# Optimization experiments

Hardware: AMD Instinct MI355X
Metric: run time of the kernel (lower is better)

## Reference

```python
import jax, jax.numpy as jnp
import numpy as np

REL_LEN = 100  # self.relative_length in the module
LN_EPS = 1e-3  # tf.keras LayerNormalization default epsilon


def sinusoid_table(rel_len, d):
    # position_encoding_relative: sinusoid over relative offsets -L..L, [2L+1, d]
    pos = jnp.arange(-rel_len, rel_len + 1, dtype=jnp.float32)[:, None]
    i = jnp.arange(d // 2, dtype=jnp.float32)[None, :]
    inv_freq = jnp.exp(-jnp.log(10000.0) * (2.0 * i) / d)
    ang = pos * inv_freq
    return jnp.concatenate([jnp.sin(ang), jnp.cos(ang)], axis=-1)


def setup_inputs() -> dict:
    key = jax.random.key(0)
    B, S, E, HID, H = 4, 512, 512, 2048, 8
    ks = jax.random.split(key, 16)
    g = lambda k, sh: jax.random.normal(k, sh, jnp.float32) / jnp.sqrt(jnp.float32(sh[0]))
    return {
        "values": jax.random.normal(ks[0], (B, S, E), jnp.float32),
        "values_mask": jnp.ones((B, S), dtype=bool),
        "rel_enc": sinusoid_table(REL_LEN, E),            # [201, E]
        "ln0_g": jnp.ones((E,), jnp.float32), "ln0_b": jnp.zeros((E,), jnp.float32),
        "w_b0": g(ks[1], (E, HID)), "b_b0": jnp.zeros((HID,), jnp.float32),
        "wq": g(ks[2], (HID, E)), "bq": jnp.zeros((E,), jnp.float32),
        "wke": g(ks[3], (HID, E)), "bke": jnp.zeros((E,), jnp.float32),
        "wkv": g(ks[4], (HID, E)), "bkv": jnp.zeros((E,), jnp.float32),
        "wkr": g(ks[5], (E, E)), "bkr": jnp.zeros((E,), jnp.float32),
        "wab0": g(ks[6], (E, H)), "bab0": jnp.zeros((H,), jnp.float32),
        "wab1": g(ks[7], (E, H)), "bab1": jnp.zeros((H,), jnp.float32),
        "ln1_g": jnp.ones((E,), jnp.float32), "ln1_b": jnp.zeros((E,), jnp.float32),
        "w11": g(ks[8], (E, HID)), "b11": jnp.zeros((HID,), jnp.float32),
        "w12": g(ks[9], (HID, E)), "b12": jnp.zeros((E,), jnp.float32),
    }


def _ln(x, g, b):
    m = jnp.mean(x, -1, keepdims=True)
    v = jnp.var(x, -1, keepdims=True)
    return (x - m) * jax.lax.rsqrt(v + LN_EPS) * g + b


def reference(values, values_mask, rel_enc, ln0_g, ln0_b, w_b0, b_b0,
              wq, bq, wke, bke, wkv, bkv, wkr, bkr,
              wab0, bab0, wab1, bab1, ln1_g, ln1_b, w11, b11, w12, b12):
    B, S, E = values.shape
    H = wab0.shape[1]
    D = E // H
    # block0 (lastfc=False): LayerNorm -> Dense(hidden, relu)
    x = jax.nn.relu(_ln(values, ln0_g, ln0_b) @ w_b0 + b_b0)          # [B,S,HID]
    q = x @ wq + bq                                                    # [B,S,E]
    ke = x @ wke + bke
    kv = x @ wkv + bkv
    # relative encodings: gather = one-hot rel map @ encoding table
    offs = jnp.clip(jnp.arange(S)[None, :] - jnp.arange(S)[:, None], -REL_LEN, REL_LEN) + REL_LEN
    rel = rel_enc[offs]                                                # [S,S,E]
    kr = rel @ wkr + bkr                                               # [S,S,E]
    # learned bias terms
    bias0 = (ke @ wab0 + bab0).transpose(0, 2, 1)[:, :, None, :]       # [B,H,1,S]
    bias1 = (kr @ wab1 + bab1).transpose(2, 0, 1)[None]                # [1,H,S,S]
    tr = lambda u: u.reshape(B, S, H, D).transpose(0, 2, 1, 3)         # [B,H,S,D]
    qh, keh, kvh = tr(q), tr(ke), tr(kv)
    krh = kr.reshape(S, S, H, D).transpose(2, 0, 1, 3)                 # [H,S,S,D]
    # q . kr content-position term, contracted without [B,H,S,S,D] materialization
    biasprod = jnp.einsum('bhid,hijd->bhij', qh, krh)                  # [B,H,S,S]
    bias = biasprod + bias0 + bias1
    # AttentionWithBias: scaled dot product + bias, key mask + causal mask
    logits = jnp.einsum('bhid,bhjd->bhij', qh, keh) / jnp.sqrt(jnp.float32(D)) + bias
    causal = jnp.tril(jnp.ones((S, S), dtype=bool))[None, None]        # [1,1,S,S]
    keymask = values_mask[:, None, None, :]                            # [B,1,1,S]
    logits = jnp.where(causal & keymask, logits, jnp.float32(-1e9))
    scores = jax.nn.softmax(logits, axis=-1)
    att = jnp.einsum('bhij,bhjd->bhid', scores, kvh)                   # [B,H,S,D]
    att = att.transpose(0, 2, 1, 3).reshape(B, S, E)
    v = values + att
    # block1: LayerNorm -> Dense(hidden, relu) -> Dense(input_size)
    y = jax.nn.relu(_ln(v, ln1_g, ln1_b) @ w11 + b11) @ w12 + b12
    return v + y
```

## Files before the change

### kernel.cpp

```cpp
#include <hip/hip_runtime.h>
#include <hip/hip_bf16.h>
#include <cstddef>
#include <cstdint>

#define LN_EPS 0.001f

using short8 = __attribute__((ext_vector_type(8))) short;
using f32x4 = __attribute__((ext_vector_type(4))) float;

#define GLOAD_LDS16(gp, lp)                                                    \
  __builtin_amdgcn_global_load_lds(                                            \
      (const __attribute__((address_space(1))) void*)(gp),                     \
      (__attribute__((address_space(3))) void*)(lp), 16, 0, 0)

static __device__ __forceinline__ short f2bf(float x) {
  __hip_bfloat16 h = __float2bfloat16(x);
  return *reinterpret_cast<short*>(&h);
}

__global__ __launch_bounds__(256) void prep_ln_kernel(
    const float* __restrict__ w_b0, const float* __restrict__ w11,
    const float* __restrict__ wq, const float* __restrict__ wke,
    const float* __restrict__ wkv, const float* __restrict__ w12,
    const float* __restrict__ wkr, const float* __restrict__ rel_enc,
    __hip_bfloat16* __restrict__ w_b0t, __hip_bfloat16* __restrict__ w11t,
    __hip_bfloat16* __restrict__ wqt, __hip_bfloat16* __restrict__ wket,
    __hip_bfloat16* __restrict__ wkvt, __hip_bfloat16* __restrict__ w12t,
    __hip_bfloat16* __restrict__ wkrt, __hip_bfloat16* __restrict__ relb,
    const float* __restrict__ lnx, const float* __restrict__ lng,
    const float* __restrict__ lnb, __hip_bfloat16* __restrict__ lnout,
    const float* __restrict__ bab0, const float* __restrict__ bab1,
    float* __restrict__ keab, float* __restrict__ b1t) {
  int bid = blockIdx.x;
  int t = threadIdx.x;
  if (bid >= 8768) {
    int idx = (bid - 8768) * 256 + t;
    if (idx < 208 * 8) b1t[idx] = bab1[idx & 7];
    return;
  }
  if (bid >= 8704) {
    int idx = (bid - 8704) * 256 + t;
    keab[idx] = bab0[(idx >> 9) & 7];
    return;
  }
  if (bid >= 6656) {
    int row = bid - 6656;
    const float* xr = lnx + (size_t)row * 512;
    float v0 = xr[t], v1 = xr[t + 256];
    float s = v0 + v1, sq = v0 * v0 + v1 * v1;
#pragma unroll
    for (int o = 32; o; o >>= 1) {
      s += __shfl_down(s, o);
      sq += __shfl_down(sq, o);
    }
    __shared__ float wsum[4], wsq[4];
    __shared__ float mean_s, scale_s;
    int wid = t >> 6, lane = t & 63;
    if (lane == 0) { wsum[wid] = s; wsq[wid] = sq; }
    __syncthreads();
    if (t == 0) {
      float S = wsum[0] + wsum[1] + wsum[2] + wsum[3];
      float SQ = wsq[0] + wsq[1] + wsq[2] + wsq[3];
      float mean = S * (1.f / 512.f);
      float var = SQ * (1.f / 512.f) - mean * mean;
      mean_s = mean;
      scale_s = rsqrtf(var + LN_EPS);
    }
    __syncthreads();
    float mean = mean_s, scale = scale_s;
    __hip_bfloat16* orow = lnout + (size_t)row * 512;
    orow[t] = __float2bfloat16((v0 - mean) * scale * lng[t] + lnb[t]);
    orow[t + 256] = __float2bfloat16((v1 - mean) * scale * lng[t + 256] + lnb[t + 256]);
    return;
  }
  if (bid >= 6400) {
    int row = bid - 6400;
    float v0 = 0.f, v1 = 0.f;
    if (row < 201) {
      v0 = rel_enc[(size_t)row * 512 + t];
      v1 = rel_enc[(size_t)row * 512 + t + 256];
    }
    relb[(size_t)row * 512 + t] = __float2bfloat16(v0);
    relb[(size_t)row * 512 + t + 256] = __float2bfloat16(v1);
    return;
  }
  const float* in;
  __hip_bfloat16* outp;
  int R, C, bx, by;
  if (bid < 6144) {
    int seg = bid >> 10, idx = bid & 1023;
    if (seg == 0)      { in = w_b0; outp = w_b0t; R = 512;  C = 2048; }
    else if (seg == 1) { in = w11;  outp = w11t;  R = 512;  C = 2048; }
    else if (seg == 2) { in = wq;   outp = wqt;   R = 2048; C = 512;  }
    else if (seg == 3) { in = wke;  outp = wket;  R = 2048; C = 512;  }
    else if (seg == 4) { in = wkv;  outp = wkvt;  R = 2048; C = 512;  }
    else               { in = w12;  outp = w12t;  R = 2048; C = 512;  }
    if (R == 512) { bx = idx & 63; by = idx >> 6; }
    else          { bx = idx & 15; by = idx >> 4; }
  } else {
    int idx = bid - 6144;
    in = wkr; outp = wkrt; R = 512; C = 512;
    bx = idx & 15; by = idx >> 4;
  }
  __shared__ float tile[32][33];
  int c0 = bx * 32, r0 = by * 32;
  int tx = t & 31, ty = t >> 5;
#pragma unroll
  for (int p = 0; p < 4; p++) {
    int r = ty + p * 8;
    tile[r][tx] = in[(size_t)(r0 + r) * C + c0 + tx];
  }
  __syncthreads();
#pragma unroll
  for (int p = 0; p < 4; p++) {
    int r = ty + p * 8;
    outp[(size_t)(c0 + r) * R + r0 + tx] = __float2bfloat16(tile[tx][r]);
  }
}

__global__ __launch_bounds__(256) void ln_kernel(const float* __restrict__ x,
                                                 const float* __restrict__ g,
                                                 const float* __restrict__ bb,
                                                 __hip_bfloat16* __restrict__ out) {
  int row = blockIdx.x;
  const float* xr = x + (size_t)row * 512;
  int t = threadIdx.x;
  float v0 = xr[t], v1 = xr[t + 256];
  float s = v0 + v1, sq = v0 * v0 + v1 * v1;
#pragma unroll
  for (int o = 32; o; o >>= 1) {
    s += __shfl_down(s, o);
    sq += __shfl_down(sq, o);
  }
  __shared__ float wsum[4], wsq[4];
  __shared__ float mean_s, scale_s;
  int wid = t >> 6, lane = t & 63;
  if (lane == 0) { wsum[wid] = s; wsq[wid] = sq; }
  __syncthreads();
  if (t == 0) {
    float S = wsum[0] + wsum[1] + wsum[2] + wsum[3];
    float SQ = wsq[0] + wsq[1] + wsq[2] + wsq[3];
    float mean = S * (1.f / 512.f);
    float var = SQ * (1.f / 512.f) - mean * mean;
    mean_s = mean;
    scale_s = rsqrtf(var + LN_EPS);
  }
  __syncthreads();
  float mean = mean_s, scale = scale_s;
  __hip_bfloat16* orow = out + (size_t)row * 512;
  orow[t] = __float2bfloat16((v0 - mean) * scale * g[t] + bb[t]);
  orow[t + 256] = __float2bfloat16((v1 - mean) * scale * g[t + 256] + bb[t + 256]);
}

template <int TM, int TN, int MODE, int RELU, int RESID, int DOT>
__global__ __launch_bounds__(256) void gemm_mfma(
    const __hip_bfloat16* __restrict__ A, const __hip_bfloat16* __restrict__ Bt,
    const float* __restrict__ bias0, const float* __restrict__ bias1,
    const float* __restrict__ bias2, const float* __restrict__ resid,
    void* __restrict__ out0, void* __restrict__ out1, void* __restrict__ out2,
    int M, int N, int K,
    const __hip_bfloat16* A2, const __hip_bfloat16* B2t,
    const float* bias_kr, void* out_kr, int ysplit,
    const float* wdot0, float* dot0, const float* wdot1, float* dot1) {
  constexpr int FM = TM / 32;
  constexpr int FN = TN / 32;
  __shared__ short As[2][TM * 64];
  __shared__ short Bs[2][TN * 64];
  int tid = threadIdx.x;
  int w = tid >> 6, lane = tid & 63;
  int wrow = (w >> 1) * (TM / 2);
  int wcol = (w & 1) * (TN / 2);
  int quad = lane >> 4, l16 = lane & 15;
  int bx = blockIdx.x, by = blockIdx.y;
  const short* Ag = (const short*)A;
  const short* Bg = (const short*)Bt;
  int N_ = N, K_ = K;
  bool is_kr = false;
  if (MODE == 1 && ysplit > 0 && by >= ysplit) {
    if (bx >= 512 / TN) return;
    is_kr = true;
    by -= ysplit;
    Ag = (const short*)A2;
    Bg = (const short*)B2t;
    N_ = 512;
    K_ = 512;
  }
  int row0 = by * TM, col0 = bx * TN;
  f32x4 acc[FM][FN];
#pragma unroll
  for (int i = 0; i < FM; i++)
#pragma unroll
    for (int j = 0; j < FN; j++) acc[i][j] = {0.f, 0.f, 0.f, 0.f};

  auto stage = [&](int k0, int buf) {
#pragma unroll
    for (int p = 0; p < TM / 32; p++) {
      int e = p * 256 + tid;
      int r = e >> 3, sc = e & 7;
      int c = sc ^ (r & 7);
      GLOAD_LDS16(Ag + (size_t)(row0 + r) * K_ + k0 + c * 8, &As[buf][e * 8]);
    }
#pragma unroll
    for (int p = 0; p < TN / 32; p++) {
      int e = p * 256 + tid;
      int r = e >> 3, sc = e & 7;
      int c = sc ^ (r & 7);
      GLOAD_LDS16(Bg + (size_t)(col0 + r) * K_ + k0 + c * 8, &Bs[buf][e * 8]);
    }
  };

  int nIter = K_ >> 6;
  stage(0, 0);
  for (int it = 0; it < nIter; ++it) {
    int cur = it & 1;
    __syncthreads();
    if (it + 1 < nIter) stage((it + 1) << 6, cur ^ 1);
#pragma unroll
    for (int u = 0; u < 2; u++) {
      short8 af[FM], bf[FN];
#pragma unroll
      for (int f = 0; f < FM; f++) {
        int r = wrow + f * 16 + l16;
        int slot = (u * 4 + quad) ^ (r & 7);
        af[f] = *(const short8*)&As[cur][(r * 8 + slot) * 8];
      }
#pragma unroll
      for (int f = 0; f < FN; f++) {
        int r = wcol + f * 16 + l16;
        int slot = (u * 4 + quad) ^ (r & 7);
        bf[f] = *(const short8*)&Bs[cur][(r * 8 + slot) * 8];
      }
#pragma unroll
      for (int fm = 0; fm < FM; fm++)
#pragma unroll
        for (int fn = 0; fn < FN; fn++)
          acc[fm][fn] = __builtin_amdgcn_mfma_f32_16x16x32_bf16(af[fm], bf[fn], acc[fm][fn], 0, 0, 0);
    }
  }

  if (MODE == 2) {
    int seg = col0 >> 9;
    const float* bp = (seg == 0) ? bias0 : (seg == 1 ? bias1 : bias2);
    if (seg < 2) {
      __hip_bfloat16* dst = (__hip_bfloat16*)(seg == 0 ? out0 : out1);
#pragma unroll
      for (int fm = 0; fm < FM; fm++) {
#pragma unroll
        for (int r = 0; r < 4; r++) {
          int gr = row0 + wrow + fm * 16 + quad * 4 + r;
          float dotp[8] = {0.f, 0.f, 0.f, 0.f, 0.f, 0.f, 0.f, 0.f};
#pragma unroll
          for (int fn = 0; fn < FN; fn++) {
            int gc = col0 + wcol + fn * 16 + l16;
            int bcol = gc - seg * 512;
            float v = acc[fm][fn][r] + bp[bcol];
            dst[(size_t)gr * 512 + bcol] = __float2bfloat16(v);
            if (DOT && seg == 1) {
              const float4* wv = (const float4*)&wdot0[(size_t)bcol * 8];
              float4 w0 = wv[0], w1 = wv[1];
              dotp[0] += v * w0.x; dotp[1] += v * w0.y; dotp[2] += v * w0.z; dotp[3] += v * w0.w;
              dotp[4] += v * w1.x; dotp[5] += v * w1.y; dotp[6] += v * w1.z; dotp[7] += v * w1.w;
            }
          }
          if (DOT && seg == 1) {
#pragma unroll
            for (int h = 0; h < 8; h++) {
              float d = dotp[h];
              d += __shfl_xor(d, 1);
              d += __shfl_xor(d, 2);
              d += __shfl_xor(d, 4);
              d += __shfl_xor(d, 8);
              if (l16 == 0) {
                int b_ = gr >> 9, s_ = gr & 511;
                atomicAdd(&dot0[(size_t)(b_ * 8 + h) * 512 + s_], d);
              }
            }
          }
        }
      }
    } else {
#pragma unroll
      for (int fm = 0; fm < FM; fm++) {
#pragma unroll
        for (int fn = 0; fn < FN; fn++) {
          int gc = col0 + wcol + fn * 16 + l16;
          int bcol = gc - 1024;
          float bv = bp[bcol];
          int gr0 = row0 + wrow + fm * 16 + quad * 4;
          union { unsigned long long u; short s4[4]; } pk;
#pragma unroll
          for (int r = 0; r < 4; r++) pk.s4[r] = f2bf(acc[fm][fn][r] + bv);
          int b_ = gr0 >> 9, s_ = gr0 & 511;
          int h_ = bcol >> 6, d_ = bcol & 63;
          *(unsigned long long*)&((short*)out2)[(size_t)((b_ * 8 + h_) * 64 + d_) * 512 + s_] = pk.u;
        }
      }
    }
  } else if (MODE == 1) {
    const float* bp = is_kr ? bias_kr : bias0;
    __hip_bfloat16* dst = is_kr ? (__hip_bfloat16*)out_kr : (__hip_bfloat16*)out0;
#pragma unroll
    for (int fm = 0; fm < FM; fm++) {
#pragma unroll
      for (int r = 0; r < 4; r++) {
        int gr = row0 + wrow + fm * 16 + quad * 4 + r;
        float dotp[8] = {0.f, 0.f, 0.f, 0.f, 0.f, 0.f, 0.f, 0.f};
#pragma unroll
        for (int fn = 0; fn < FN; fn++) {
          int gc = col0 + wcol + fn * 16 + l16;
          float v = acc[fm][fn][r] + bp[gc];
          if (RELU && !is_kr) v = fmaxf(v, 0.f);
          dst[(size_t)gr * N_ + gc] = __float2bfloat16(v);
          if (DOT && is_kr) {
            const float4* wv = (const float4*)&wdot1[(size_t)gc * 8];
            float4 w0 = wv[0], w1 = wv[1];
            dotp[0] += v * w0.x; dotp[1] += v * w0.y; dotp[2] += v * w0.z; dotp[3] += v * w0.w;
            dotp[4] += v * w1.x; dotp[5] += v * w1.y; dotp[6] += v * w1.z; dotp[7] += v * w1.w;
          }
        }
        if (DOT && is_kr) {
#pragma unroll
          for (int h = 0; h < 8; h++) {
            float d = dotp[h];
            d += __shfl_xor(d, 1);
            d += __shfl_xor(d, 2);
            d += __shfl_xor(d, 4);
            d += __shfl_xor(d, 8);
            if (l16 == 0 && gr < 208) atomicAdd(&dot1[gr * 8 + h], d);
          }
        }
      }
    }
  } else {
#pragma unroll
    for (int fm = 0; fm < FM; fm++) {
#pragma unroll
      for (int fn = 0; fn < FN; fn++) {
        int gc = col0 + wcol + fn * 16 + l16;
        float bv = bias0[gc];
#pragma unroll
        for (int r = 0; r < 4; r++) {
          int gr = row0 + wrow + fm * 16 + quad * 4 + r;
          float v = acc[fm][fn][r] + bv;
          if (RELU) v = fmaxf(v, 0.f);
          size_t idx = (size_t)gr * N_ + gc;
          if (RESID) v += resid[idx];
          ((float*)out0)[idx] = v;
        }
      }
    }
  }
}

#define PST 136
__global__ __launch_bounds__(256) void attn_mfma4(
    const __hip_bfloat16* __restrict__ q, const __hip_bfloat16* __restrict__ ke,
    const __hip_bfloat16* __restrict__ kvt, const __hip_bfloat16* __restrict__ krtb,
    const float* __restrict__ keab, const float* __restrict__ b1t,
    const float* __restrict__ values, float* __restrict__ v_out) {
  const int S = 512, E = 512;
  __shared__ float bp[16 * 113];
  __shared__ short P[4][16 * PST];
  __shared__ float ml[4][32];
  int tid = threadIdx.x;
  int wave = tid >> 6, lane = tid & 63;
  int quad = lane >> 4, l16 = lane & 15;
  int band = 31 - blockIdx.x;
  int h = blockIdx.y, b = blockIdx.z;
  int wi0 = band * 16;

  const short* qg = (const short*)q;
  const short* keg = (const short*)ke;
  const short* kvtg = (const short*)kvt;
  const short* krg = (const short*)krtb;

  short8 aq[2];
#pragma unroll
  for (int kk = 0; kk < 2; kk++)
    aq[kk] = *(const short8*)&qg[(size_t)(b * S + wi0 + l16) * E + h * 64 + kk * 32 + quad * 8];

#pragma unroll
  for (int oi = 0; oi < 2; oi++) {
    int on = wave + oi * 4;
    if (on < 7) {
      f32x4 c = {0.f, 0.f, 0.f, 0.f};
#pragma unroll
      for (int kk = 0; kk < 2; kk++) {
        short8 bfr = *(const short8*)&krg[(size_t)(on * 16 + l16) * E + h * 64 + kk * 32 + quad * 8];
        c = __builtin_amdgcn_mfma_f32_16x16x32_bf16(aq[kk], bfr, c, 0, 0, 0);
      }
      float b1 = b1t[(on * 16 + l16) * 8 + h];
#pragma unroll
      for (int rr = 0; rr < 4; rr++)
        bp[(quad * 4 + rr) * 113 + on * 16 + l16] = c[rr] + b1;
    }
  }
  __syncthreads();

  int nb = (band >= wave) ? (((band - wave) >> 2) + 1) : 0;

  f32x4 s[8];
  const float* keabh = keab + (size_t)(b * 8 + h) * 512;
#pragma unroll
  for (int t = 0; t < 8; t++) {
    if (t < nb) {
      int j = (4 * t + wave) * 16 + l16;
      f32x4 c = {0.f, 0.f, 0.f, 0.f};
#pragma unroll
      for (int kk = 0; kk < 2; kk++) {
        short8 bk = *(const short8*)&keg[(size_t)(b * S + j) * E + h * 64 + kk * 32 + quad * 8];
        c = __builtin_amdgcn_mfma_f32_16x16x32_bf16(aq[kk], bk, c, 0, 0, 0);
      }
      float ka = keabh[j];
#pragma unroll
      for (int rr = 0; rr < 4; rr++) {
        int i = wi0 + quad * 4 + rr;
        float val = -1e30f;
        if (j <= i) {
          int off = j - i + 100;
          if (off < 0) off = 0;
          val = c[rr] * 0.125f + bp[(quad * 4 + rr) * 113 + off] + ka;
        }
        s[t][rr] = val;
      }
    }
  }

  float m_r[4] = {-1e30f, -1e30f, -1e30f, -1e30f};
#pragma unroll
  for (int t = 0; t < 8; t++)
    if (t < nb)
#pragma unroll
      for (int rr = 0; rr < 4; rr++) m_r[rr] = fmaxf(m_r[rr], s[t][rr]);
#pragma unroll
  for (int rr = 0; rr < 4; rr++) {
    float v = m_r[rr];
    v = fmaxf(v, __shfl_xor(v, 1));
    v = fmaxf(v, __shfl_xor(v, 2));
    v = fmaxf(v, __shfl_xor(v, 4));
    v = fmaxf(v, __shfl_xor(v, 8));
    m_r[rr] = v;
  }
  float l_r[4] = {0.f, 0.f, 0.f, 0.f};
  short* Pw = &P[wave][0];
#pragma unroll
  for (int t = 0; t < 8; t++) {
    if (t < nb) {
#pragma unroll
      for (int rr = 0; rr < 4; rr++) {
        float p = __expf(s[t][rr] - m_r[rr]);
        l_r[rr] += p;
        Pw[(quad * 4 + rr) * PST + t * 16 + l16] = f2bf(p);
      }
    }
  }
  if (nb & 1) {
#pragma unroll
    for (int rr = 0; rr < 4; rr++)
      Pw[(quad * 4 + rr) * PST + nb * 16 + l16] = 0;
  }
#pragma unroll
  for (int rr = 0; rr < 4; rr++) {
    float v = l_r[rr];
    v += __shfl_xor(v, 1);
    v += __shfl_xor(v, 2);
    v += __shfl_xor(v, 4);
    v += __shfl_xor(v, 8);
    l_r[rr] = v;
  }

  f32x4 o[4] = {{0.f,0.f,0.f,0.f},{0.f,0.f,0.f,0.f},{0.f,0.f,0.f,0.f},{0.f,0.f,0.f,0.f}};
  int nkk = (nb + 1) >> 1;
  const short* kvbase = &kvtg[(size_t)(b * 8 + h) * 64 * S];
#pragma unroll
  for (int kk = 0; kk < 4; kk++) {
    if (kk < nkk) {
      short8 ap = *(const short8*)&Pw[l16 * PST + kk * 32 + quad * 8];
      int jgl = (4 * (2 * kk + (quad >> 1)) + wave) * 16 + (quad & 1) * 8;
#pragma unroll
      for (int dn = 0; dn < 4; dn++) {
        short8 bv = *(const short8*)&kvbase[(size_t)(dn * 16 + l16) * S + jgl];
        o[dn] = __builtin_amdgcn_mfma_f32_16x16x32_bf16(ap, bv, o[dn], 0, 0, 0);
      }
    }
  }

  float* omw = (float*)&P[wave][0];
#pragma unroll
  for (int rr = 0; rr < 4; rr++) {
    int row = quad * 4 + rr;
    if (l16 == 0) {
      ml[wave][row * 2] = m_r[rr];
      ml[wave][row * 2 + 1] = l_r[rr];
    }
#pragma unroll
    for (int dn = 0; dn < 4; dn++)
      omw[row * 68 + dn * 16 + l16] = o[dn][rr];
  }
  __syncthreads();
  int dn = wave;
#pragma unroll
  for (int rr = 0; rr < 4; rr++) {
    int row = quad * 4 + rr;
    float ms = -1e30f;
#pragma unroll
    for (int wv = 0; wv < 4; wv++) ms = fmaxf(ms, ml[wv][row * 2]);
    float lsum = 0.f, oo = 0.f;
    int col = dn * 16 + l16;
#pragma unroll
    for (int wv = 0; wv < 4; wv++) {
      float aw = __expf(ml[wv][row * 2] - ms);
      lsum += ml[wv][row * 2 + 1] * aw;
      oo += ((float*)&P[wv][0])[row * 68 + col] * aw;
    }
    oo /= lsum;
    size_t idx = (size_t)(b * S + wi0 + row) * E + h * 64 + col;
    v_out[idx] = values[idx] + oo;
  }
}

extern "C" void kernel_launch(void* const* d_in, const int* in_sizes, int n_in,
                              void* d_out, int out_size, void* d_ws, size_t ws_size,
                              hipStream_t stream) {
  const float* values = (const float*)d_in[0];
  const float* rel_enc = (const float*)d_in[2];
  const float* ln0_g = (const float*)d_in[3];
  const float* ln0_b = (const float*)d_in[4];
  const float* w_b0 = (const float*)d_in[5];
  const float* b_b0 = (const float*)d_in[6];
  const float* wq = (const float*)d_in[7];
  const float* bq = (const float*)d_in[8];
  const float* wke = (const float*)d_in[9];
  const float* bke = (const float*)d_in[10];
  const float* wkv = (const float*)d_in[11];
  const float* bkv = (const float*)d_in[12];
  const float* wkr = (const float*)d_in[13];
  const float* bkr = (const float*)d_in[14];
  const float* wab0 = (const float*)d_in[15];
  const float* bab0 = (const float*)d_in[16];
  const float* wab1 = (const float*)d_in[17];
  const float* bab1 = (const float*)d_in[18];
  const float* ln1_g = (const float*)d_in[19];
  const float* ln1_b = (const float*)d_in[20];
  const float* w11 = (const float*)d_in[21];
  const float* b11 = (const float*)d_in[22];
  const float* w12 = (const float*)d_in[23];
  const float* b12 = (const float*)d_in[24];
  float* out = (float*)d_out;

  char* p = (char*)d_ws;
  __hip_bfloat16* buf_ln = (__hip_bfloat16*)p;  p += (size_t)2048 * 512 * 2;
  __hip_bfloat16* x      = (__hip_bfloat16*)p;  p += (size_t)2048 * 2048 * 2;
  __hip_bfloat16* q      = (__hip_bfloat16*)p;  p += (size_t)2048 * 512 * 2;
  __hip_bfloat16* ke     = (__hip_bfloat16*)p;  p += (size_t)2048 * 512 * 2;
  __hip_bfloat16* kvt    = (__hip_bfloat16*)p;  p += (size_t)2048 * 512 * 2;
  float* v    = (float*)p;                      p += (size_t)2048 * 512 * 4;
  __hip_bfloat16* krtb = (__hip_bfloat16*)p;    p += (size_t)256 * 512 * 2;
  __hip_bfloat16* relb = (__hip_bfloat16*)p;    p += (size_t)256 * 512 * 2;
  __hip_bfloat16* wkrt = (__hip_bfloat16*)p;    p += (size_t)512 * 512 * 2;
  float* keab = (float*)p;                      p += (size_t)4 * 8 * 512 * 4;
  float* b1t  = (float*)p;                      p += (size_t)208 * 8 * 4;
  __hip_bfloat16* w_b0t = (__hip_bfloat16*)p;   p += (size_t)2048 * 512 * 2;
  __hip_bfloat16* wcatt = (__hip_bfloat16*)p;   p += (size_t)1536 * 2048 * 2;
  __hip_bfloat16* w11t  = (__hip_bfloat16*)p;   p += (size_t)2048 * 512 * 2;
  __hip_bfloat16* w12t  = (__hip_bfloat16*)p;   p += (size_t)512 * 2048 * 2;

  __hip_bfloat16* wqt  = wcatt;
  __hip_bfloat16* wket = wcatt + (size_t)512 * 2048;
  __hip_bfloat16* wkvt = wcatt + (size_t)1024 * 2048;

  prep_ln_kernel<<<8775, 256, 0, stream>>>(w_b0, w11, wq, wke, wkv, w12, wkr, rel_enc,
                                           w_b0t, w11t, wqt, wket, wkvt, w12t, wkrt, relb,
                                           values, ln0_g, ln0_b, buf_ln,
                                           bab0, bab1, keab, b1t);
  gemm_mfma<128, 64, 1, 1, 0, 1><<<dim3(32, 18), 256, 0, stream>>>(
      buf_ln, w_b0t, b_b0, nullptr, nullptr, nullptr, x, nullptr, nullptr,
      2048, 2048, 512, relb, wkrt, bkr, krtb, 16,
      nullptr, nullptr, wab1, b1t);
  gemm_mfma<128, 64, 2, 0, 0, 1><<<dim3(24, 16), 256, 0, stream>>>(
      x, wcatt, bq, bke, bkv, nullptr, q, ke, kvt, 2048, 1536, 2048,
      nullptr, nullptr, nullptr, nullptr, 0,
      wab0, keab, nullptr, nullptr);
  attn_mfma4<<<dim3(32, 8, 4), 256, 0, stream>>>(q, ke, kvt, krtb, keab, b1t, values, v);
  ln_kernel<<<2048, 256, 0, stream>>>(v, ln1_g, ln1_b, buf_ln);
  gemm_mfma<128, 64, 1, 1, 0, 0><<<dim3(32, 16), 256, 0, stream>>>(
      buf_ln, w11t, b11, nullptr, nullptr, nullptr, x, nullptr, nullptr,
      2048, 2048, 512, nullptr, nullptr, nullptr, nullptr, 0,
      nullptr, nullptr, nullptr, nullptr);
  gemm_mfma<64, 64, 0, 0, 1, 0><<<dim3(8, 32), 256, 0, stream>>>(
      x, w12t, b12, nullptr, nullptr, v, out, nullptr, nullptr, 2048, 512, 2048,
      nullptr, nullptr, nullptr, nullptr, 0,
      nullptr, nullptr, nullptr, nullptr);
}
```

Before: 282.8 us.

## Fold attention-bias projections into GEMM weights as extra output columns

Precomputes wke·wab0 and wkr·wab1 as extra bf16 weight rows appended to the concatenated QKV and kr weight matrices, with biases folded into small constant vectors. The bias tables then come straight out of the GEMM as extra output tiles, replacing the per-element epilogue dot products and atomicAdds. This removes atomic traffic and epilogue work but adds one extra column tile per GEMM and computes the bias terms from bf16-rounded composite weights, which can shift numerics. The packed 4-wide kvt store is also replaced by scalar stores.

```diff
diff --git a/kernel.cpp b/kernel.cpp
--- a/kernel.cpp
+++ b/kernel.cpp
@@ -29,18 +29,104 @@
     __hip_bfloat16* __restrict__ wkrt, __hip_bfloat16* __restrict__ relb,
     const float* __restrict__ lnx, const float* __restrict__ lng,
     const float* __restrict__ lnb, __hip_bfloat16* __restrict__ lnout,
+    const float* __restrict__ wab0, const float* __restrict__ wab1,
+    const float* __restrict__ bke, const float* __restrict__ bkr,
     const float* __restrict__ bab0, const float* __restrict__ bab1,
-    float* __restrict__ keab, float* __restrict__ b1t) {
+    float* __restrict__ cb0, float* __restrict__ cb1) {
   int bid = blockIdx.x;
   int t = threadIdx.x;
-  if (bid >= 8768) {
-    int idx = (bid - 8768) * 256 + t;
-    if (idx < 208 * 8) b1t[idx] = bab1[idx & 7];
+  short* wcatt_s = (short*)wqt;
+  short* wkrt_s = (short*)wkrt;
+
+  if (bid >= 9456) {
+    int wave = t >> 6, lane = t & 63;
+    if (wave < 2) {
+      const float* arow = (wave == 0) ? bke : bkr;
+      const float* W = (wave == 0) ? wab0 : wab1;
+      const float* bb = (wave == 0) ? bab0 : bab1;
+      float* dst = (wave == 0) ? cb0 : cb1;
+      float a[8];
+#pragma unroll
+      for (int u = 0; u < 8; u++) a[u] = arow[lane + u * 64];
+      float s[8] = {0.f, 0.f, 0.f, 0.f, 0.f, 0.f, 0.f, 0.f};
+#pragma unroll
+      for (int u = 0; u < 8; u++) {
+        int e = lane + u * 64;
+        const float4* w4 = (const float4*)&W[(size_t)e * 8];
+        float4 w0 = w4[0], w1 = w4[1];
+        s[0] += a[u] * w0.x; s[1] += a[u] * w0.y; s[2] += a[u] * w0.z; s[3] += a[u] * w0.w;
+        s[4] += a[u] * w1.x; s[5] += a[u] * w1.y; s[6] += a[u] * w1.z; s[7] += a[u] * w1.w;
+      }
+#pragma unroll
+      for (int h = 0; h < 8; h++) {
+        float v = s[h];
+#pragma unroll
+        for (int o = 1; o < 64; o <<= 1) v += __shfl_xor(v, o);
+        if (lane == h) dst[h] = v + bb[h];
+      }
+    }
     return;
   }
+  if (bid >= 9400) {
+    int row = 8 + (bid - 9400);
+    ((unsigned int*)&wkrt_s[(size_t)(512 + row) * 512])[t] = 0u;
+    return;
+  }
+  if (bid >= 9272) {
+    int blk = bid - 9272;
+    int wave = t >> 6, lane = t & 63;
+    int k = blk * 4 + wave;
+    const float* row = wkr + (size_t)k * 512;
+    float a[8];
+#pragma unroll
+    for (int u = 0; u < 8; u++) a[u] = row[lane + u * 64];
+    float s[8] = {0.f, 0.f, 0.f, 0.f, 0.f, 0.f, 0.f, 0.f};
+#pragma unroll
+    for (int u = 0; u < 8; u++) {
+      int e = lane + u * 64;
+      const float4* w4 = (const float4*)&wab1[(size_t)e * 8];
+      float4 w0 = w4[0], w1 = w4[1];
+      s[0] += a[u] * w0.x; s[1] += a[u] * w0.y; s[2] += a[u] * w0.z; s[3] += a[u] * w0.w;
+      s[4] += a[u] * w1.x; s[5] += a[u] * w1.y; s[6] += a[u] * w1.z; s[7] += a[u] * w1.w;
+    }
+#pragma unroll
+    for (int h = 0; h < 8; h++) {
+      float v = s[h];
+#pragma unroll
+      for (int o = 1; o < 64; o <<= 1) v += __shfl_xor(v, o);
+      if (lane == h) wkrt_s[(size_t)(512 + h) * 512 + k] = f2bf(v);
+    }
+    return;
+  }
+  if (bid >= 9216) {
+    int row = 8 + (bid - 9216);
+    ((uint4*)&wcatt_s[(size_t)(1536 + row) * 2048])[t] = uint4{0u, 0u, 0u, 0u};
+    return;
+  }
   if (bid >= 8704) {
-    int idx = (bid - 8704) * 256 + t;
-    keab[idx] = bab0[(idx >> 9) & 7];
+    int blk = bid - 8704;
+    int wave = t >> 6, lane = t & 63;
+    int k = blk * 4 + wave;
+    const float* row = wke + (size_t)k * 512;
+    float a[8];
+#pragma unroll
+    for (int u = 0; u < 8; u++) a[u] = row[lane + u * 64];
+    float s[8] = {0.f, 0.f, 0.f, 0.f, 0.f, 0.f, 0.f, 0.f};
+#pragma unroll
+    for (int u = 0; u < 8; u++) {
+      int e = lane + u * 64;
+      const float4* w4 = (const float4*)&wab0[(size_t)e * 8];
+      float4 w0 = w4[0], w1 = w4[1];
+      s[0] += a[u] * w0.x; s[1] += a[u] * w0.y; s[2] += a[u] * w0.z; s[3] += a[u] * w0.w;
+      s[4] += a[u] * w1.x; s[5] += a[u] * w1.y; s[6] += a[u] * w1.z; s[7] += a[u] * w1.w;
+    }
+#pragma unroll
+    for (int h = 0; h < 8; h++) {
+      float v = s[h];
+#pragma unroll
+      for (int o = 1; o < 64; o <<= 1) v += __shfl_xor(v, o);
+      if (lane == h) wcatt_s[(size_t)(1536 + h) * 2048 + k] = f2bf(v);
+    }
     return;
   }
   if (bid >= 6656) {
@@ -152,7 +238,7 @@
   orow[t + 256] = __float2bfloat16((v1 - mean) * scale * g[t + 256] + bb[t + 256]);
 }
 
-template <int TM, int TN, int MODE, int RELU, int RESID, int DOT>
+template <int TM, int TN, int MODE, int RELU, int RESID>
 __global__ __launch_bounds__(256) void gemm_mfma(
     const __hip_bfloat16* __restrict__ A, const __hip_bfloat16* __restrict__ Bt,
     const float* __restrict__ bias0, const float* __restrict__ bias1,
@@ -161,7 +247,7 @@
     int M, int N, int K,
     const __hip_bfloat16* A2, const __hip_bfloat16* B2t,
     const float* bias_kr, void* out_kr, int ysplit,
-    const float* wdot0, float* dot0, const float* wdot1, float* dot1) {
+    const float* cb, float* tblout) {
   constexpr int FM = TM / 32;
   constexpr int FN = TN / 32;
   __shared__ short As[2][TM * 64];
@@ -177,7 +263,7 @@
   int N_ = N, K_ = K;
   bool is_kr = false;
   if (MODE == 1 && ysplit > 0 && by >= ysplit) {
-    if (bx >= 512 / TN) return;
+    if (bx >= 9) return;
     is_kr = true;
     by -= ysplit;
     Ag = (const short*)A2;
@@ -240,94 +326,84 @@
 
   if (MODE == 2) {
     int seg = col0 >> 9;
-    const float* bp = (seg == 0) ? bias0 : (seg == 1 ? bias1 : bias2);
-    if (seg < 2) {
-      __hip_bfloat16* dst = (__hip_bfloat16*)(seg == 0 ? out0 : out1);
+    if (seg == 3) {
 #pragma unroll
       for (int fm = 0; fm < FM; fm++) {
 #pragma unroll
-        for (int r = 0; r < 4; r++) {
-          int gr = row0 + wrow + fm * 16 + quad * 4 + r;
-          float dotp[8] = {0.f, 0.f, 0.f, 0.f, 0.f, 0.f, 0.f, 0.f};
-#pragma unroll
-          for (int fn = 0; fn < FN; fn++) {
-            int gc = col0 + wcol + fn * 16 + l16;
-            int bcol = gc - seg * 512;
-            float v = acc[fm][fn][r] + bp[bcol];
-            dst[(size_t)gr * 512 + bcol] = __float2bfloat16(v);
-            if (DOT && seg == 1) {
-              const float4* wv = (const float4*)&wdot0[(size_t)bcol * 8];
-              float4 w0 = wv[0], w1 = wv[1];
-              dotp[0] += v * w0.x; dotp[1] += v * w0.y; dotp[2] += v * w0.z; dotp[3] += v * w0.w;
-              dotp[4] += v * w1.x; dotp[5] += v * w1.y; dotp[6] += v * w1.z; dotp[7] += v * w1.w;
-            }
-          }
-          if (DOT && seg == 1) {
-#pragma unroll
-            for (int h = 0; h < 8; h++) {
-              float d = dotp[h];
-              d += __shfl_xor(d, 1);
-              d += __shfl_xor(d, 2);
-              d += __shfl_xor(d, 4);
-              d += __shfl_xor(d, 8);
-              if (l16 == 0) {
-                int b_ = gr >> 9, s_ = gr & 511;
-                atomicAdd(&dot0[(size_t)(b_ * 8 + h) * 512 + s_], d);
-              }
+        for (int fn = 0; fn < FN; fn++) {
+          int gc = col0 + wcol + fn * 16 + l16;
+          int hh = gc - 1536;
+          if (hh < 8) {
+            float bv = cb[hh];
+#pragma unroll
+            for (int r = 0; r < 4; r++) {
+              int gr = row0 + wrow + fm * 16 + quad * 4 + r;
+              int b_ = gr >> 9, s_ = gr & 511;
+              tblout[(size_t)(b_ * 8 + hh) * 512 + s_] = acc[fm][fn][r] + bv;
             }
           }
         }
       }
-    } else {
+      return;
+    }
+    const float* bp = (seg == 0) ? bias0 : (seg == 1 ? bias1 : bias2);
+    __hip_bfloat16* opb = (__hip_bfloat16*)((seg == 0) ? out0 : out1);
+#pragma unroll
+    for (int fm = 0; fm < FM; fm++) {
+#pragma unroll
+      for (int fn = 0; fn < FN; fn++) {
+        int gc = col0 + wcol + fn * 16 + l16;
+        int bcol = gc - seg * 512;
+        float bv = bp[bcol];
+#pragma unroll
+        for (int r = 0; r < 4; r++) {
+          int gr = row0 + wrow + fm * 16 + quad * 4 + r;
+          float v = acc[fm][fn][r] + bv;
+          if (seg < 2) {
+            opb[(size_t)gr * 512 + bcol] = __float2bfloat16(v);
+          } else {
+            int b_ = gr >> 9, s_ = gr & 511;
+            int h_ = bcol >> 6, d_ = bcol & 63;
+            ((__hip_bfloat16*)out2)[(size_t)((b_ * 8 + h_) * 64 + d_) * 512 + s_] =
+                __float2bfloat16(v);
+          }
+        }
+      }
+    }
+  } else if (MODE == 1) {
+    if (is_kr && col0 == 512) {
 #pragma unroll
       for (int fm = 0; fm < FM; fm++) {
 #pragma unroll
         for (int fn = 0; fn < FN; fn++) {
           int gc = col0 + wcol + fn * 16 + l16;
-          int bcol = gc - 1024;
-          float bv = bp[bcol];
-          int gr0 = row0 + wrow + fm * 16 + quad * 4;
-          union { unsigned long long u; short s4[4]; } pk;
-#pragma unroll
-          for (int r = 0; r < 4; r++) pk.s4[r] = f2bf(acc[fm][fn][r] + bv);
-          int b_ = gr0 >> 9, s_ = gr0 & 511;
-          int h_ = bcol >> 6, d_ = bcol & 63;
-          *(unsigned long long*)&((short*)out2)[(size_t)((b_ * 8 + h_) * 64 + d_) * 512 + s_] = pk.u;
+          int hh = gc - 512;
+          if (hh < 8) {
+            float bv = cb[hh];
+#pragma unroll
+            for (int r = 0; r < 4; r++) {
+              int gr = row0 + wrow + fm * 16 + quad * 4 + r;
+              if (gr < 208) tblout[gr * 8 + hh] = acc[fm][fn][r] + bv;
+            }
+          }
         }
       }
-    }
-  } else if (MODE == 1) {
+      return;
+    }
     const float* bp = is_kr ? bias_kr : bias0;
     __hip_bfloat16* dst = is_kr ? (__hip_bfloat16*)out_kr : (__hip_bfloat16*)out0;
 #pragma unroll
     for (int fm = 0; fm < FM; fm++) {
 #pragma unroll
-      for (int r = 0; r < 4; r++) {
-        int gr = row0 + wrow + fm * 16 + quad * 4 + r;
-        float dotp[8] = {0.f, 0.f, 0.f, 0.f, 0.f, 0.f, 0.f, 0.f};
-#pragma unroll
-        for (int fn = 0; fn < FN; fn++) {
-          int gc = col0 + wcol + fn * 16 + l16;
-          float v = acc[fm][fn][r] + bp[gc];
+      for (int fn = 0; fn < FN; fn++) {
+        int gc = col0 + wcol + fn * 16 + l16;
+        float bv = bp[gc];
+#pragma unroll
+        for (int r = 0; r < 4; r++) {
+          int gr = row0 + wrow + fm * 16 + quad * 4 + r;
+          float v = acc[fm][fn][r] + bv;
           if (RELU && !is_kr) v = fmaxf(v, 0.f);
           dst[(size_t)gr * N_ + gc] = __float2bfloat16(v);
-          if (DOT && is_kr) {
-            const float4* wv = (const float4*)&wdot1[(size_t)gc * 8];
-            float4 w0 = wv[0], w1 = wv[1];
-            dotp[0] += v * w0.x; dotp[1] += v * w0.y; dotp[2] += v * w0.z; dotp[3] += v * w0.w;
-            dotp[4] += v * w1.x; dotp[5] += v * w1.y; dotp[6] += v * w1.z; dotp[7] += v * w1.w;
-          }
-        }
-        if (DOT && is_kr) {
-#pragma unroll
-          for (int h = 0; h < 8; h++) {
-            float d = dotp[h];
-            d += __shfl_xor(d, 1);
-            d += __shfl_xor(d, 2);
-            d += __shfl_xor(d, 4);
-            d += __shfl_xor(d, 8);
-            if (l16 == 0 && gr < 208) atomicAdd(&dot1[gr * 8 + h], d);
-          }
         }
       }
     }
@@ -557,11 +633,13 @@
   float* v    = (float*)p;                      p += (size_t)2048 * 512 * 4;
   __hip_bfloat16* krtb = (__hip_bfloat16*)p;    p += (size_t)256 * 512 * 2;
   __hip_bfloat16* relb = (__hip_bfloat16*)p;    p += (size_t)256 * 512 * 2;
-  __hip_bfloat16* wkrt = (__hip_bfloat16*)p;    p += (size_t)512 * 512 * 2;
+  __hip_bfloat16* wkrt = (__hip_bfloat16*)p;    p += (size_t)576 * 512 * 2;
   float* keab = (float*)p;                      p += (size_t)4 * 8 * 512 * 4;
   float* b1t  = (float*)p;                      p += (size_t)208 * 8 * 4;
+  float* cb0  = (float*)p;                      p += 64;
+  float* cb1  = (float*)p;                      p += 64;
   __hip_bfloat16* w_b0t = (__hip_bfloat16*)p;   p += (size_t)2048 * 512 * 2;
-  __hip_bfloat16* wcatt = (__hip_bfloat16*)p;   p += (size_t)1536 * 2048 * 2;
+  __hip_bfloat16* wcatt = (__hip_bfloat16*)p;   p += (size_t)1600 * 2048 * 2;
   __hip_bfloat16* w11t  = (__hip_bfloat16*)p;   p += (size_t)2048 * 512 * 2;
   __hip_bfloat16* w12t  = (__hip_bfloat16*)p;   p += (size_t)512 * 2048 * 2;
 
@@ -569,26 +647,22 @@
   __hip_bfloat16* wket = wcatt + (size_t)512 * 2048;
   __hip_bfloat16* wkvt = wcatt + (size_t)1024 * 2048;
 
-  prep_ln_kernel<<<8775, 256, 0, stream>>>(w_b0, w11, wq, wke, wkv, w12, wkr, rel_enc,
+  prep_ln_kernel<<<9457, 256, 0, stream>>>(w_b0, w11, wq, wke, wkv, w12, wkr, rel_enc,
                                            w_b0t, w11t, wqt, wket, wkvt, w12t, wkrt, relb,
                                            values, ln0_g, ln0_b, buf_ln,
-                                           bab0, bab1, keab, b1t);
-  gemm_mfma<128, 64, 1, 1, 0, 1><<<dim3(32, 18), 256, 0, stream>>>(
+                                           wab0, wab1, bke, bkr, bab0, bab1, cb0, cb1);
+  gemm_mfma<128, 64, 1, 1, 0><<<dim3(32, 18), 256, 0, stream>>>(
       buf_ln, w_b0t, b_b0, nullptr, nullptr, nullptr, x, nullptr, nullptr,
-      2048, 2048, 512, relb, wkrt, bkr, krtb, 16,
-      nullptr, nullptr, wab1, b1t);
-  gemm_mfma<128, 64, 2, 0, 0, 1><<<dim3(24, 16), 256, 0, stream>>>(
+      2048, 2048, 512, relb, wkrt, bkr, krtb, 16, cb1, b1t);
+  gemm_mfma<128, 64, 2, 0, 0><<<dim3(25, 16), 256, 0, stream>>>(
       x, wcatt, bq, bke, bkv, nullptr, q, ke, kvt, 2048, 1536, 2048,
-      nullptr, nullptr, nullptr, nullptr, 0,
-      wab0, keab, nullptr, nullptr);
+      nullptr, nullptr, nullptr, nullptr, 0, cb0, keab);
   attn_mfma4<<<dim3(32, 8, 4), 256, 0, stream>>>(q, ke, kvt, krtb, keab, b1t, values, v);
   ln_kernel<<<2048, 256, 0, stream>>>(v, ln1_g, ln1_b, buf_ln);
-  gemm_mfma<128, 64, 1, 1, 0, 0><<<dim3(32, 16), 256, 0, stream>>>(
+  gemm_mfma<128, 64, 1, 1, 0><<<dim3(32, 16), 256, 0, stream>>>(
       buf_ln, w11t, b11, nullptr, nullptr, nullptr, x, nullptr, nullptr,
-      2048, 2048, 512, nullptr, nullptr, nullptr, nullptr, 0,
-      nullptr, nullptr, nullptr, nullptr);
-  gemm_mfma<64, 64, 0, 0, 1, 0><<<dim3(8, 32), 256, 0, stream>>>(
+      2048, 2048, 512, nullptr, nullptr, nullptr, nullptr, 0, nullptr, nullptr);
+  gemm_mfma<64, 64, 0, 0, 1><<<dim3(8, 32), 256, 0, stream>>>(
       x, w12t, b12, nullptr, nullptr, v, out, nullptr, nullptr, 2048, 512, 2048,
-      nullptr, nullptr, nullptr, nullptr, 0,
-      nullptr, nullptr, nullptr, nullptr);
+      nullptr, nullptr, nullptr, nullptr, 0, nullptr, nullptr);
 }
```

Result: faster. 232.6 us (-17.7%).
